# Kernel tuning notes

Measured on AMD Instinct MI355X. Metric: run time of the kernel, lower is better.

## Reference

```python
import jax, jax.numpy as jnp
import numpy as np

DIM = 192
HEADS = 6
H = 64
W = 64
B = 16
HID = int(DIM * 4.0)


def make_rope(Hh, Ww, c):
    # mirrors torch RoPE buffer: k_max = c // (2*2), angles (H,W,c//2)
    k_max = c // 4
    theta = 1.0 / (10000.0 ** (np.arange(k_max) / k_max))
    hi = np.arange(Hh)[:, None, None] * theta  # (H,1,k)
    wi = np.arange(Ww)[None, :, None] * theta  # (1,W,k)
    angles = np.concatenate([np.broadcast_to(hi, (Hh, Ww, k_max)),
                             np.broadcast_to(wi, (Hh, Ww, k_max))], axis=-1)
    return jnp.asarray(np.cos(angles), jnp.float32), jnp.asarray(np.sin(angles), jnp.float32)


def rope_apply(x, cos, sin):
    # x: (b,H,W,c); complex multiply on (re,im) pairs along last dim
    b, Hh, Ww, c = x.shape
    xr = x.reshape(b, Hh, Ww, c // 2, 2)
    re, im = xr[..., 0], xr[..., 1]
    out = jnp.stack([re * cos - im * sin, re * sin + im * cos], axis=-1)
    return out.reshape(b, Hh, Ww, c)


def dwconv(x, w, b):
    # depthwise 3x3, NCHW, kernel (C,1,3,3)
    C = x.shape[1]
    y = jax.lax.conv_general_dilated(x, w, (1, 1), 'SAME',
                                     dimension_numbers=('NCHW', 'OIHW', 'NCHW'),
                                     feature_group_count=C)
    return y + b[None, :, None, None]


def conv1x1(x, w, b):
    return jnp.einsum('bchw,oc->bohw', x, w) + b[None, :, None, None]


def ln2d(x, w, b):
    # LayerNorm over channel dim at each spatial location
    mu = x.mean(axis=1, keepdims=True)
    var = x.var(axis=1, keepdims=True)
    xn = (x - mu) / jnp.sqrt(var + 1e-5)
    return xn * w[None, :, None, None] + b[None, :, None, None]


def setup_inputs() -> dict:
    key = jax.random.key(0)
    ks = jax.random.split(key, 32)
    s = 0.02
    def p(i, shape):
        return jax.random.normal(ks[i], shape, jnp.float32) * s
    return {
        'x': jax.random.normal(ks[0], (B, DIM, H, W), jnp.float32),
        'cpe1_w': p(1, (DIM, 1, 3, 3)), 'cpe1_b': p(2, (DIM,)),
        'norm1_w': jnp.ones((DIM,), jnp.float32), 'norm1_b': jnp.zeros((DIM,), jnp.float32),
        'act_proj_w': p(3, (DIM, DIM)), 'act_proj_b': p(4, (DIM,)),
        'in_proj_w': p(5, (DIM, DIM)), 'in_proj_b': p(6, (DIM,)),
        'dwc_w': p(7, (DIM, 1, 3, 3)), 'dwc_b': p(8, (DIM,)),
        'qk_w': p(9, (2 * DIM, DIM)), 'qk_b': p(10, (2 * DIM,)),
        'lepe_w': p(11, (DIM, 1, 3, 3)), 'lepe_b': p(12, (DIM,)),
        'out_proj_w': p(13, (DIM, DIM)), 'out_proj_b': p(14, (DIM,)),
        'cpe2_w': p(15, (DIM, 1, 3, 3)), 'cpe2_b': p(16, (DIM,)),
        'norm2_w': jnp.ones((DIM,), jnp.float32), 'norm2_b': jnp.zeros((DIM,), jnp.float32),
        'fc1_w': p(17, (HID, DIM)), 'fc1_b': p(18, (HID,)),
        'fc2_w': p(19, (DIM, HID)), 'fc2_b': p(20, (DIM,)),
    }


def reference(x, cpe1_w, cpe1_b, norm1_w, norm1_b, act_proj_w, act_proj_b,
              in_proj_w, in_proj_b, dwc_w, dwc_b, qk_w, qk_b, lepe_w, lepe_b,
              out_proj_w, out_proj_b, cpe2_w, cpe2_b, norm2_w, norm2_b,
              fc1_w, fc1_b, fc2_w, fc2_b):
    b, c, Hh, Ww = x.shape
    n = Hh * Ww
    d = c // HEADS
    cos, sin = make_rope(Hh, Ww, c)

    # x = x + cpe1(x)
    x = x + dwconv(x, cpe1_w, cpe1_b)

    # MLLA block on norm1(x)
    y = ln2d(x, norm1_w, norm1_b)
    act_res = jax.nn.silu(conv1x1(y, act_proj_w, act_proj_b))
    y = conv1x1(y, in_proj_w, in_proj_b)
    t = jax.nn.silu(dwconv(y, dwc_w, dwc_b)).transpose(0, 2, 3, 1).reshape(b, n, c)

    # linear attention with ELU+1 feature map, RoPE, LePE
    qk = t @ qk_w.T + qk_b
    q = jax.nn.elu(qk[..., :c]) + 1.0
    k = jax.nn.elu(qk[..., c:]) + 1.0
    v = t
    q_rope = rope_apply(q.reshape(b, Hh, Ww, c), cos, sin).reshape(b, n, HEADS, d).transpose(0, 2, 1, 3)
    k_rope = rope_apply(k.reshape(b, Hh, Ww, c), cos, sin).reshape(b, n, HEADS, d).transpose(0, 2, 1, 3)
    qh = q.reshape(b, n, HEADS, d).transpose(0, 2, 1, 3)
    kh = k.reshape(b, n, HEADS, d).transpose(0, 2, 1, 3)
    vh = v.reshape(b, n, HEADS, d).transpose(0, 2, 1, 3)
    kmean = kh.mean(axis=2, keepdims=True)  # (b,h,1,d)
    z = 1.0 / (jnp.einsum('bhnd,bhmd->bhnm', qh, kmean) + 1e-6)  # (b,h,n,1)
    scale = n ** -0.5
    kv = jnp.einsum('bhnd,bhne->bhde', k_rope * scale, vh * scale)  # (b,h,d,d)
    attn = jnp.einsum('bhnd,bhde->bhne', q_rope, kv) * z  # (b,h,n,d)
    attn = attn.transpose(0, 2, 1, 3).reshape(b, n, c)
    v_img = vh.transpose(0, 2, 1, 3).reshape(b, Hh, Ww, c).transpose(0, 3, 1, 2)
    lepe = dwconv(v_img, lepe_w, lepe_b).transpose(0, 2, 3, 1).reshape(b, n, c)
    attn = attn + lepe

    y = attn.transpose(0, 2, 1).reshape(b, c, Hh, Ww)
    y = conv1x1(y * act_res, out_proj_w, out_proj_b)
    x = x + y

    # x = x + cpe2(x)
    x = x + dwconv(x, cpe2_w, cpe2_b)

    # MLP on norm2(x)
    y = ln2d(x, norm2_w, norm2_b)
    y = conv1x1(y, fc1_w, fc1_b)
    y = jax.nn.gelu(y, approximate=False)
    y = conv1x1(y, fc2_w, fc2_b)
    return x + y
```

## Files before the change

kernel.cpp:

```cpp
#include <hip/hip_runtime.h>
#include <hip/hip_bf16.h>

#define BQ 16
#define CH 192
#define HH 64
#define WW 64
#define HWSZ 4096
#define NPIX 65536
#define NHEADS 6
#define HDIM 32
#define NPAIR 96
#define KMAXR 48
#define HID 768

typedef __hip_bfloat16 bf16;
typedef __attribute__((ext_vector_type(8))) short short8;
typedef __attribute__((ext_vector_type(4))) float floatx4;

static __device__ __forceinline__ float b2f(bf16 v) { return __bfloat162float(v); }
static __device__ __forceinline__ bf16 f2b(float v) { return __float2bfloat16(v); }

static __device__ __forceinline__ float4 ld4(const float* p) { return *(const float4*)p; }
static __device__ __forceinline__ float4 ld4(const bf16* p) {
  uint2 u = *(const uint2*)p;
  return make_float4(__uint_as_float(u.x << 16), __uint_as_float(u.x & 0xffff0000u),
                     __uint_as_float(u.y << 16), __uint_as_float(u.y & 0xffff0000u));
}

template <int ACT>
static __device__ __forceinline__ float actf(float v) {
  if (ACT == 1) return v / (1.f + expf(-v));
  if (ACT == 2) return (v > 0.f) ? v + 1.f : expf(v);
  if (ACT == 3) return 0.5f * v * (1.f + erff(v * 0.70710678118654752f));
  return v;
}
static __device__ __forceinline__ void stv(float* p, float v) { *p = v; }
static __device__ __forceinline__ void stv(bf16* p, float v) { *p = __float2bfloat16(v); }

__global__ __launch_bounds__(256) void k_transpose_in(const float* __restrict__ in,
                                                      float* __restrict__ out) {
  __shared__ float tile[32][33];
  int c0 = blockIdx.x * 32, hw0 = blockIdx.y * 32, b = blockIdx.z;
  int tx = threadIdx.x, ty = threadIdx.y;
  const float* src = in + (size_t)b * CH * HWSZ;
  #pragma unroll
  for (int j = 0; j < 32; j += 8)
    tile[ty + j][tx] = src[(size_t)(c0 + ty + j) * HWSZ + hw0 + tx];
  __syncthreads();
  float* dst = out + (size_t)b * HWSZ * CH;
  #pragma unroll
  for (int j = 0; j < 32; j += 8)
    dst[(size_t)(hw0 + ty + j) * CH + c0 + tx] = tile[tx][ty + j];
}

__global__ __launch_bounds__(256) void k_transpose_out(const float* __restrict__ in,
                                                       float* __restrict__ out) {
  __shared__ float tile[32][33];
  int c0 = blockIdx.x * 32, hw0 = blockIdx.y * 32, b = blockIdx.z;
  int tx = threadIdx.x, ty = threadIdx.y;
  const float* src = in + (size_t)b * HWSZ * CH;
  #pragma unroll
  for (int j = 0; j < 32; j += 8)
    tile[ty + j][tx] = src[(size_t)(hw0 + ty + j) * CH + c0 + tx];
  __syncthreads();
  float* dst = out + (size_t)b * CH * HWSZ;
  #pragma unroll
  for (int j = 0; j < 32; j += 8)
    dst[(size_t)(c0 + ty + j) * HWSZ + hw0 + tx] = tile[tx][ty + j];
}

__global__ __launch_bounds__(256) void k_rope(float* __restrict__ cosT, float* __restrict__ sinT) {
  int i = blockIdx.x * 256 + threadIdx.x;
  if (i >= NPAIR * HWSZ) return;
  int hw = i & (HWSZ - 1);
  int p = i >> 12;
  int h = hw >> 6, w = hw & 63;
  int j = (p < KMAXR) ? p : p - KMAXR;
  float theta = powf(10000.f, -(float)j / (float)KMAXR);
  float pos = (p < KMAXR) ? (float)h : (float)w;
  float ang = pos * theta;
  cosT[i] = cosf(ang);
  sinT[i] = sinf(ang);
}

template <typename TI>
__global__ __launch_bounds__(192) void k_cpe_ln(const TI* __restrict__ in,
                                                const float* __restrict__ w,
                                                const float* __restrict__ bias,
                                                const float* __restrict__ g,
                                                const float* __restrict__ bt,
                                                float* __restrict__ x1o,
                                                bf16* __restrict__ yo) {
  __shared__ float grs[12][4], grq[12][4];
  int t = threadIdx.x;
  int cg = t % 48, st = t / 48;
  int c0 = cg * 4;
  int gpix = blockIdx.x * 16 + st * 4;
  int hw = gpix & (HWSZ - 1);
  int h = hw >> 6, wx = hw & 63;
  float4 w4[9];
  #pragma unroll
  for (int i = 0; i < 9; i++) w4[i] = ld4(w + c0 * 9 + i * 4);
  const float* wf = (const float*)w4;
  float4 bi = ld4(bias + c0);
  float4 acc[4];
  #pragma unroll
  for (int i = 0; i < 4; i++) acc[i] = bi;
  const TI* base = in + (size_t)gpix * CH + c0;
  #pragma unroll
  for (int dh = -1; dh <= 1; dh++) {
    bool rv = ((unsigned)(h + dh) < HH);
    float4 tap[6];
    #pragma unroll
    for (int c = 0; c < 6; c++) {
      int col = wx - 1 + c;
      bool v = rv && ((unsigned)col < WW);
      tap[c] = v ? ld4(base + (dh * WW + (c - 1)) * CH) : make_float4(0, 0, 0, 0);
    }
    #pragma unroll
    for (int i = 0; i < 4; i++) {
      #pragma unroll
      for (int dw = 0; dw < 3; dw++) {
        const int tp = (dh + 1) * 3 + dw;
        float4 tv = tap[i + dw];
        acc[i].x += tv.x * wf[0 * 9 + tp];
        acc[i].y += tv.y * wf[1 * 9 + tp];
        acc[i].z += tv.z * wf[2 * 9 + tp];
        acc[i].w += tv.w * wf[3 * 9 + tp];
      }
      if (dh == 0) {
        acc[i].x += tap[i + 1].x;
        acc[i].y += tap[i + 1].y;
        acc[i].z += tap[i + 1].z;
        acc[i].w += tap[i + 1].w;
      }
    }
  }
  float s4[4], q4[4];
  #pragma unroll
  for (int i = 0; i < 4; i++) {
    *(float4*)&x1o[(size_t)(gpix + i) * CH + c0] = acc[i];
    s4[i] = acc[i].x + acc[i].y + acc[i].z + acc[i].w;
    q4[i] = acc[i].x * acc[i].x + acc[i].y * acc[i].y + acc[i].z * acc[i].z +
            acc[i].w * acc[i].w;
  }
  #pragma unroll
  for (int m = 1; m <= 8; m <<= 1) {
    #pragma unroll
    for (int i = 0; i < 4; i++) {
      s4[i] += __shfl_xor(s4[i], m, 64);
      q4[i] += __shfl_xor(q4[i], m, 64);
    }
  }
  if ((t & 15) == 0) {
    #pragma unroll
    for (int i = 0; i < 4; i++) { grs[t >> 4][i] = s4[i]; grq[t >> 4][i] = q4[i]; }
  }
  __syncthreads();
  int s3 = st * 3;
  float4 gg = ld4(g + c0);
  float4 bb = ld4(bt + c0);
  #pragma unroll
  for (int i = 0; i < 4; i++) {
    float S = grs[s3][i] + grs[s3 + 1][i] + grs[s3 + 2][i];
    float SS = grq[s3][i] + grq[s3 + 1][i] + grq[s3 + 2][i];
    float mu = S * (1.f / CH);
    float inv = rsqrtf(SS * (1.f / CH) - mu * mu + 1e-5f);
    __align__(8) bf16 tmp[4] = {f2b((acc[i].x - mu) * inv * gg.x + bb.x),
                                f2b((acc[i].y - mu) * inv * gg.y + bb.y),
                                f2b((acc[i].z - mu) * inv * gg.z + bb.z),
                                f2b((acc[i].w - mu) * inv * gg.w + bb.w)};
    *(uint2*)&yo[(size_t)(gpix + i) * CH + c0] = *(uint2*)tmp;
  }
}

template <int MODE>
__global__ __launch_bounds__(192) void k_dwconv_strip(const bf16* __restrict__ in,
                                                      const float* __restrict__ w,
                                                      const float* __restrict__ bias,
                                                      bf16* __restrict__ out) {
  int t = threadIdx.x;
  int cg = t % 48, st = t / 48;
  int c0 = cg * 4;
  int gpix = blockIdx.x * 16 + st * 4;
  int hw = gpix & (HWSZ - 1);
  int h = hw >> 6, wx = hw & 63;
  float4 w4[9];
  #pragma unroll
  for (int i = 0; i < 9; i++) w4[i] = ld4(w + c0 * 9 + i * 4);
  const float* wf = (const float*)w4;
  float4 bi = ld4(bias + c0);
  float4 acc[4];
  #pragma unroll
  for (int i = 0; i < 4; i++) acc[i] = bi;
  const bf16* base = in + (size_t)gpix * CH + c0;
  #pragma unroll
  for (int dh = -1; dh <= 1; dh++) {
    bool rv = ((unsigned)(h + dh) < HH);
    float4 tap[6];
    #pragma unroll
    for (int c = 0; c < 6; c++) {
      int col = wx - 1 + c;
      bool v = rv && ((unsigned)col < WW);
      tap[c] = v ? ld4(base + (dh * WW + (c - 1)) * CH) : make_float4(0, 0, 0, 0);
    }
    #pragma unroll
    for (int i = 0; i < 4; i++) {
      #pragma unroll
      for (int dw = 0; dw < 3; dw++) {
        const int tp = (dh + 1) * 3 + dw;
        float4 tv = tap[i + dw];
        acc[i].x += tv.x * wf[0 * 9 + tp];
        acc[i].y += tv.y * wf[1 * 9 + tp];
        acc[i].z += tv.z * wf[2 * 9 + tp];
        acc[i].w += tv.w * wf[3 * 9 + tp];
      }
    }
  }
  #pragma unroll
  for (int i = 0; i < 4; i++) {
    bf16* op = out + (size_t)(gpix + i) * CH + c0;
    float a0 = acc[i].x, a1 = acc[i].y, a2 = acc[i].z, a3 = acc[i].w;
    if (MODE == 1) {
      a0 = a0 / (1.f + expf(-a0));
      a1 = a1 / (1.f + expf(-a1));
      a2 = a2 / (1.f + expf(-a2));
      a3 = a3 / (1.f + expf(-a3));
    } else {
      float4 cur = ld4(op);
      a0 += cur.x; a1 += cur.y; a2 += cur.z; a3 += cur.w;
    }
    __align__(8) bf16 tmp[4] = {f2b(a0), f2b(a1), f2b(a2), f2b(a3)};
    *(uint2*)op = *(uint2*)tmp;
  }
}

template <int ACT, int MULA, int RES, typename TO>
__global__ __launch_bounds__(256) void k_gemm(const bf16* __restrict__ A,
                                              const bf16* __restrict__ A2,
                                              const float* __restrict__ Wt,
                                              const float* __restrict__ bias,
                                              const float* __restrict__ Rsd,
                                              TO* __restrict__ Cout,
                                              int M, int N, int K) {
  __shared__ bf16 As[128][40];
  __shared__ bf16 Bs[64][40];
  int t = threadIdx.x;
  int wave = t >> 6, lane = t & 63;
  int quad = lane >> 4, l16 = lane & 15;
  int m0 = blockIdx.x * 128, n0 = blockIdx.y * 64;
  floatx4 acc[2][4] = {};
  for (int k0 = 0; k0 < K; k0 += 32) {
    #pragma unroll
    for (int i = 0; i < 2; i++) {
      int idx = t + i * 256;
      int m = idx >> 2, kk = (idx & 3) * 8;
      const bf16* pa = &A[(size_t)(m0 + m) * K + k0 + kk];
      if (!MULA) {
        *(short8*)&As[m][kk] = *(const short8*)pa;
      } else {
        const bf16* pb = &A2[(size_t)(m0 + m) * K + k0 + kk];
        __align__(16) bf16 tmp[8];
        #pragma unroll
        for (int j = 0; j < 8; j++) tmp[j] = f2b(b2f(pa[j]) * b2f(pb[j]));
        *(short8*)&As[m][kk] = *(const short8*)tmp;
      }
    }
    #pragma unroll
    for (int i = 0; i < 2; i++) {
      int idx = t + i * 256;
      int n = idx >> 3, kk = (idx & 7) * 4;
      float4 v = *(const float4*)&Wt[(size_t)(n0 + n) * K + k0 + kk];
      __align__(8) bf16 tmp[4] = {f2b(v.x), f2b(v.y), f2b(v.z), f2b(v.w)};
      *(uint2*)&Bs[n][kk] = *(uint2*)tmp;
    }
    __syncthreads();
    short8 af[2], bfr[4];
    #pragma unroll
    for (int i = 0; i < 2; i++)
      af[i] = *(const short8*)&As[wave * 32 + i * 16 + l16][quad * 8];
    #pragma unroll
    for (int j = 0; j < 4; j++)
      bfr[j] = *(const short8*)&Bs[j * 16 + l16][quad * 8];
    #pragma unroll
    for (int i = 0; i < 2; i++)
      #pragma unroll
      for (int j = 0; j < 4; j++)
        acc[i][j] = __builtin_amdgcn_mfma_f32_16x16x32_bf16(af[i], bfr[j], acc[i][j], 0, 0, 0);
    __syncthreads();
  }
  #pragma unroll
  for (int i = 0; i < 2; i++) {
    #pragma unroll
    for (int j = 0; j < 4; j++) {
      int n = n0 + j * 16 + l16;
      float bn = bias[n];
      #pragma unroll
      for (int r = 0; r < 4; r++) {
        int m = m0 + wave * 32 + i * 16 + quad * 4 + r;
        float v = actf<ACT>(acc[i][j][r] + bn);
        if (RES) v += Rsd[(size_t)m * N + n];
        stv(&Cout[(size_t)m * N + n], v);
      }
    }
  }
}

template <int ACTA, int ACTB, int KMEAN>
__global__ __launch_bounds__(256) void k_gemm_dual(const bf16* __restrict__ A,
                                                   const float* __restrict__ WtA,
                                                   const float* __restrict__ biasA,
                                                   const float* __restrict__ WtB,
                                                   const float* __restrict__ biasB,
                                                   bf16* __restrict__ OutA,
                                                   bf16* __restrict__ OutB,
                                                   float* __restrict__ KM,
                                                   int K) {
  __shared__ bf16 As[128][40];
  __shared__ bf16 Bs[64][40];
  __shared__ float colsum[64];
  int t = threadIdx.x;
  int wave = t >> 6, lane = t & 63;
  int quad = lane >> 4, l16 = lane & 15;
  int m0 = blockIdx.x * 128, n0 = blockIdx.y * 64;
  int half = n0 >= 192;
  int n0l = half ? n0 - 192 : n0;
  const float* Wt = half ? WtB : WtA;
  const float* bias = half ? biasB : biasA;
  bf16* Out = half ? OutB : OutA;
  if (KMEAN && half && t < 64) colsum[t] = 0.f;
  floatx4 acc[2][4] = {};
  for (int k0 = 0; k0 < K; k0 += 32) {
    #pragma unroll
    for (int i = 0; i < 2; i++) {
      int idx = t + i * 256;
      int m = idx >> 2, kk = (idx & 3) * 8;
      *(short8*)&As[m][kk] = *(const short8*)&A[(size_t)(m0 + m) * K + k0 + kk];
    }
    #pragma unroll
    for (int i = 0; i < 2; i++) {
      int idx = t + i * 256;
      int n = idx >> 3, kk = (idx & 7) * 4;
      float4 v = *(const float4*)&Wt[(size_t)(n0l + n) * K + k0 + kk];
      __align__(8) bf16 tmp[4] = {f2b(v.x), f2b(v.y), f2b(v.z), f2b(v.w)};
      *(uint2*)&Bs[n][kk] = *(uint2*)tmp;
    }
    __syncthreads();
    short8 af[2], bfr[4];
    #pragma unroll
    for (int i = 0; i < 2; i++)
      af[i] = *(const short8*)&As[wave * 32 + i * 16 + l16][quad * 8];
    #pragma unroll
    for (int j = 0; j < 4; j++)
      bfr[j] = *(const short8*)&Bs[j * 16 + l16][quad * 8];
    #pragma unroll
    for (int i = 0; i < 2; i++)
      #pragma unroll
      for (int j = 0; j < 4; j++)
        acc[i][j] = __builtin_amdgcn_mfma_f32_16x16x32_bf16(af[i], bfr[j], acc[i][j], 0, 0, 0);
    __syncthreads();
  }
  #pragma unroll
  for (int j = 0; j < 4; j++) {
    int nl = n0l + j * 16 + l16;
    float bn = bias[nl];
    float csum = 0.f;
    #pragma unroll
    for (int i = 0; i < 2; i++) {
      #pragma unroll
      for (int r = 0; r < 4; r++) {
        int m = m0 + wave * 32 + i * 16 + quad * 4 + r;
        float v = half ? actf<ACTB>(acc[i][j][r] + bn) : actf<ACTA>(acc[i][j][r] + bn);
        if (KMEAN && half) csum += v;
        Out[(size_t)m * CH + nl] = f2b(v);
      }
    }
    if (KMEAN && half) atomicAdd(&colsum[j * 16 + l16], csum);
  }
  if (KMEAN && half) {
    __syncthreads();
    if (t < 64) {
      int b = m0 >> 12;
      atomicAdd(&KM[b * CH + n0l + t], colsum[t] * (1.f / 4096.f));
    }
  }
}

__global__ __launch_bounds__(256) void k_kv(const bf16* __restrict__ k,
                                            const bf16* __restrict__ v,
                                            const float* __restrict__ cosT,
                                            const float* __restrict__ sinT,
                                            float* __restrict__ kv) {
  int bh = blockIdx.x;
  int b = bh / NHEADS, hd = bh % NHEADS;
  int chunk0 = blockIdx.y * 512;
  __shared__ bf16 ks[256][40];
  __shared__ bf16 vs[256][40];
  int t = threadIdx.x;
  int d = t >> 3;
  int e0 = (t & 7) * 4;
  float a0 = 0, a1 = 0, a2 = 0, a3 = 0;
  for (int sub = 0; sub < 2; sub++) {
    int n0 = chunk0 + sub * 256;
    #pragma unroll
    for (int it = 0; it < 4; it++) {
      int idx = t + it * 256;
      int row = idx >> 2, c0 = (idx & 3) * 8;
      int n = n0 + row;
      size_t gi = ((size_t)(b * HWSZ + n)) * CH + hd * HDIM + c0;
      *(short8*)&vs[row][c0] = *(const short8*)&v[gi];
      float4 klo = ld4(&k[gi]);
      float4 khi = ld4(&k[gi + 4]);
      int prb = hd * 16 + (c0 >> 1);
      float cs0 = cosT[(size_t)(prb + 0) * HWSZ + n];
      float sn0 = sinT[(size_t)(prb + 0) * HWSZ + n];
      float cs1 = cosT[(size_t)(prb + 1) * HWSZ + n];
      float sn1 = sinT[(size_t)(prb + 1) * HWSZ + n];
      float cs2 = cosT[(size_t)(prb + 2) * HWSZ + n];
      float sn2 = sinT[(size_t)(prb + 2) * HWSZ + n];
      float cs3 = cosT[(size_t)(prb + 3) * HWSZ + n];
      float sn3 = sinT[(size_t)(prb + 3) * HWSZ + n];
      __align__(16) bf16 kt[8];
      kt[0] = f2b(klo.x * cs0 - klo.y * sn0);
      kt[1] = f2b(klo.x * sn0 + klo.y * cs0);
      kt[2] = f2b(klo.z * cs1 - klo.w * sn1);
      kt[3] = f2b(klo.z * sn1 + klo.w * cs1);
      kt[4] = f2b(khi.x * cs2 - khi.y * sn2);
      kt[5] = f2b(khi.x * sn2 + khi.y * cs2);
      kt[6] = f2b(khi.z * cs3 - khi.w * sn3);
      kt[7] = f2b(khi.z * sn3 + khi.w * cs3);
      *(short8*)&ks[row][c0] = *(const short8*)kt;
    }
    __syncthreads();
    #pragma unroll 4
    for (int i = 0; i < 256; i++) {
      float kd = b2f(ks[i][d]);
      float4 vv = ld4(&vs[i][e0]);
      a0 += kd * vv.x;
      a1 += kd * vv.y;
      a2 += kd * vv.z;
      a3 += kd * vv.w;
    }
    __syncthreads();
  }
  float* dst = kv + (size_t)bh * (HDIM * HDIM) + d * HDIM + e0;
  const float sc = 1.f / 4096.f;
  atomicAdd(dst + 0, a0 * sc);
  atomicAdd(dst + 1, a1 * sc);
  atomicAdd(dst + 2, a2 * sc);
  atomicAdd(dst + 3, a3 * sc);
}

__global__ __launch_bounds__(256) void k_attn(const bf16* __restrict__ q,
                                              const float* __restrict__ kv,
                                              const float* __restrict__ kmean,
                                              const float* __restrict__ cosT,
                                              const float* __restrict__ sinT,
                                              bf16* __restrict__ attn) {
  int hd = blockIdx.y, b = blockIdx.z;
  int hw = blockIdx.x * 256 + threadIdx.x;
  int bh = b * NHEADS + hd;
  __shared__ float kvs[32][33];
  __shared__ float kms[32];
  #pragma unroll
  for (int i = 0; i < 4; i++) {
    int idx = threadIdx.x + i * 256;
    kvs[idx >> 5][idx & 31] = kv[(size_t)bh * 1024 + idx];
  }
  if (threadIdx.x < 32) kms[threadIdx.x] = kmean[b * CH + hd * HDIM + threadIdx.x];
  __syncthreads();
  int pix = b * HWSZ + hw;
  const bf16* qp = q + (size_t)pix * CH + hd * HDIM;
  float qv[32];
  #pragma unroll
  for (int i = 0; i < 32; i++) qv[i] = b2f(qp[i]);
  float z = 1e-6f;
  #pragma unroll
  for (int d = 0; d < 32; d++) z += qv[d] * kms[d];
  float o[32] = {};
  #pragma unroll
  for (int p = 0; p < 16; p++) {
    float cs = cosT[(size_t)(hd * 16 + p) * HWSZ + hw];
    float sn = sinT[(size_t)(hd * 16 + p) * HWSZ + hw];
    float re = qv[2 * p], im = qv[2 * p + 1];
    float qr = re * cs - im * sn;
    float qi = re * sn + im * cs;
    #pragma unroll
    for (int e = 0; e < 32; e++)
      o[e] += qr * kvs[2 * p][e] + qi * kvs[2 * p + 1][e];
  }
  float zi = 1.f / z;
  bf16* op = attn + (size_t)pix * CH + hd * HDIM;
  #pragma unroll
  for (int i = 0; i < 4; i++) {
    __align__(16) bf16 tmp[8];
    #pragma unroll
    for (int j = 0; j < 8; j++) tmp[j] = f2b(o[i * 8 + j] * zi);
    *(short8*)&op[i * 8] = *(const short8*)tmp;
  }
}

extern "C" void kernel_launch(void* const* d_in, const int* in_sizes, int n_in,
                              void* d_out, int out_size, void* d_ws, size_t ws_size,
                              hipStream_t stream) {
  const float* x = (const float*)d_in[0];
  const float* cpe1w = (const float*)d_in[1];
  const float* cpe1b = (const float*)d_in[2];
  const float* n1w = (const float*)d_in[3];
  const float* n1b = (const float*)d_in[4];
  const float* apw = (const float*)d_in[5];
  const float* apb = (const float*)d_in[6];
  const float* ipw = (const float*)d_in[7];
  const float* ipb = (const float*)d_in[8];
  const float* dwcw = (const float*)d_in[9];
  const float* dwcb = (const float*)d_in[10];
  const float* qkw = (const float*)d_in[11];
  const float* qkb = (const float*)d_in[12];
  const float* lepw = (const float*)d_in[13];
  const float* lepb = (const float*)d_in[14];
  const float* opw = (const float*)d_in[15];
  const float* opb = (const float*)d_in[16];
  const float* cpe2w = (const float*)d_in[17];
  const float* cpe2b = (const float*)d_in[18];
  const float* n2w = (const float*)d_in[19];
  const float* n2b = (const float*)d_in[20];
  const float* f1w = (const float*)d_in[21];
  const float* f1b = (const float*)d_in[22];
  const float* f2w = (const float*)d_in[23];
  const float* f2b = (const float*)d_in[24];
  float* out = (float*)d_out;

  float* ws = (float*)d_ws;
  const size_t S = (size_t)NPIX * CH;
  float* FA = ws;
  float* FB = ws + S;
  bf16* barena = (bf16*)(ws + 2 * S);
  bf16* b0 = barena;
  bf16* b1 = barena + S;
  bf16* b2 = barena + 2 * S;
  bf16* KB = (bf16*)FA;
  float* COS = ws + 2 * S + 3 * S / 2;
  float* SIN = COS + (size_t)NPAIR * HWSZ;
  float* KV = SIN + (size_t)NPAIR * HWSZ;
  float* KM = KV + BQ * NHEADS * HDIM * HDIM;
  bf16* HIDB = (bf16*)FB;

  dim3 tb(32, 8);
  k_transpose_in<<<dim3(6, 128, BQ), tb, 0, stream>>>(x, FA);
  k_rope<<<dim3(NPAIR * HWSZ / 256), dim3(256), 0, stream>>>(COS, SIN);
  k_cpe_ln<float><<<dim3(NPIX / 16), dim3(192), 0, stream>>>(FA, cpe1w, cpe1b, n1w, n1b, FB, b0);
  k_gemm_dual<1, 0, 0><<<dim3(NPIX / 128, 6), dim3(256), 0, stream>>>(
      b0, apw, apb, ipw, ipb, b1, b2, nullptr, CH);
  k_dwconv_strip<1><<<dim3(NPIX / 16), dim3(192), 0, stream>>>(b2, dwcw, dwcb, b0);
  hipMemsetAsync(KM, 0, (size_t)BQ * CH * sizeof(float), stream);
  k_gemm_dual<2, 2, 1><<<dim3(NPIX / 128, 6), dim3(256), 0, stream>>>(
      b0, qkw, qkb, qkw + CH * CH, qkb + CH, b2, KB, KM, CH);
  hipMemsetAsync(KV, 0, (size_t)BQ * NHEADS * HDIM * HDIM * sizeof(float), stream);
  k_kv<<<dim3(BQ * NHEADS, 8), dim3(256), 0, stream>>>(KB, b0, COS, SIN, KV);
  k_attn<<<dim3(HWSZ / 256, NHEADS, BQ), dim3(256), 0, stream>>>(b2, KV, KM, COS, SIN, KB);
  k_dwconv_strip<2><<<dim3(NPIX / 16), dim3(192), 0, stream>>>(b0, lepw, lepb, KB);
  k_gemm<0, 1, 1, bf16><<<dim3(NPIX / 128, 3), dim3(256), 0, stream>>>(
      KB, b1, opw, opb, FB, b2, NPIX, CH, CH);
  k_cpe_ln<bf16><<<dim3(NPIX / 16), dim3(192), 0, stream>>>(b2, cpe2w, cpe2b, n2w, n2b, FA, b0);
  for (int s = 0; s < 2; s++) {
    size_t off = (size_t)s * (NPIX / 2) * CH;
    k_gemm<3, 0, 0, bf16><<<dim3((NPIX / 2) / 128, HID / 64), dim3(256), 0, stream>>>(
        b0 + off, (const bf16*)nullptr, f1w, f1b, (const float*)nullptr, HIDB, NPIX / 2, HID, CH);
    k_gemm<0, 0, 1, float><<<dim3((NPIX / 2) / 128, 3), dim3(256), 0, stream>>>(
        HIDB, (const bf16*)nullptr, f2w, f2b, FA + off, FA + off, NPIX / 2, CH, HID);
  }
  k_transpose_out<<<dim3(6, 128, BQ), tb, 0, stream>>>(FA, out);
}
```

Before: 633.9 us.

## Pre-convert weights to bf16 once and stage full 192-wide K chunks in GEMMs

Adds a kernel that converts all linear weights to bf16 in workspace once per call, so GEMMs load bf16 weights directly instead of converting fp32 per tile. The GEMM kernels now stage 192-wide K slices into LDS (the whole K for dual GEMMs) and run six MFMA steps per barrier, cutting syncs and load-loop overhead. LDS per block grows to about 77 KB, which may lower occupancy, and one extra small kernel launch is added.

Result: no change. 637.3 us (+0.5%).

```diff
diff --git a/kernel.cpp b/kernel.cpp
--- a/kernel.cpp
+++ b/kernel.cpp
@@ -81,6 +81,29 @@
   float ang = pos * theta;
   cosT[i] = cosf(ang);
   sinT[i] = sinf(ang);
+}
+
+#define WTOT 479232
+__global__ __launch_bounds__(256) void k_wcvt(const float* __restrict__ ap,
+                                              const float* __restrict__ ip,
+                                              const float* __restrict__ qk,
+                                              const float* __restrict__ op,
+                                              const float* __restrict__ f1,
+                                              const float* __restrict__ f2,
+                                              bf16* __restrict__ o) {
+  int i = (blockIdx.x * 256 + threadIdx.x) * 4;
+  if (i >= WTOT) return;
+  const float* src;
+  int off;
+  if (i < 36864)       { src = ap; off = 0; }
+  else if (i < 73728)  { src = ip; off = 36864; }
+  else if (i < 147456) { src = qk; off = 73728; }
+  else if (i < 184320) { src = op; off = 147456; }
+  else if (i < 331776) { src = f1; off = 184320; }
+  else                 { src = f2; off = 331776; }
+  float4 v = ld4(src + (i - off));
+  __align__(8) bf16 t4[4] = {f2b(v.x), f2b(v.y), f2b(v.z), f2b(v.w)};
+  *(uint2*)&o[i] = *(uint2*)t4;
 }
 
 template <typename TI>
@@ -238,55 +261,56 @@
 template <int ACT, int MULA, int RES, typename TO>
 __global__ __launch_bounds__(256) void k_gemm(const bf16* __restrict__ A,
                                               const bf16* __restrict__ A2,
-                                              const float* __restrict__ Wt,
+                                              const bf16* __restrict__ Wt,
                                               const float* __restrict__ bias,
                                               const float* __restrict__ Rsd,
                                               TO* __restrict__ Cout,
                                               int M, int N, int K) {
-  __shared__ bf16 As[128][40];
-  __shared__ bf16 Bs[64][40];
+  __shared__ bf16 As[128][200];
+  __shared__ bf16 Bs[64][200];
   int t = threadIdx.x;
   int wave = t >> 6, lane = t & 63;
   int quad = lane >> 4, l16 = lane & 15;
   int m0 = blockIdx.x * 128, n0 = blockIdx.y * 64;
   floatx4 acc[2][4] = {};
-  for (int k0 = 0; k0 < K; k0 += 32) {
-    #pragma unroll
-    for (int i = 0; i < 2; i++) {
+  for (int kc = 0; kc < K; kc += 192) {
+    #pragma unroll
+    for (int i = 0; i < 12; i++) {
       int idx = t + i * 256;
-      int m = idx >> 2, kk = (idx & 3) * 8;
-      const bf16* pa = &A[(size_t)(m0 + m) * K + k0 + kk];
+      int m = idx / 24, ck = (idx % 24) * 8;
+      const bf16* pa = &A[(size_t)(m0 + m) * K + kc + ck];
       if (!MULA) {
-        *(short8*)&As[m][kk] = *(const short8*)pa;
+        *(short8*)&As[m][ck] = *(const short8*)pa;
       } else {
-        const bf16* pb = &A2[(size_t)(m0 + m) * K + k0 + kk];
+        const bf16* pb = &A2[(size_t)(m0 + m) * K + kc + ck];
         __align__(16) bf16 tmp[8];
         #pragma unroll
         for (int j = 0; j < 8; j++) tmp[j] = f2b(b2f(pa[j]) * b2f(pb[j]));
-        *(short8*)&As[m][kk] = *(const short8*)tmp;
+        *(short8*)&As[m][ck] = *(const short8*)tmp;
       }
     }
     #pragma unroll
-    for (int i = 0; i < 2; i++) {
+    for (int i = 0; i < 6; i++) {
       int idx = t + i * 256;
-      int n = idx >> 3, kk = (idx & 7) * 4;
-      float4 v = *(const float4*)&Wt[(size_t)(n0 + n) * K + k0 + kk];
-      __align__(8) bf16 tmp[4] = {f2b(v.x), f2b(v.y), f2b(v.z), f2b(v.w)};
-      *(uint2*)&Bs[n][kk] = *(uint2*)tmp;
+      int n = idx / 24, ck = (idx % 24) * 8;
+      *(short8*)&Bs[n][ck] = *(const short8*)&Wt[(size_t)(n0 + n) * K + kc + ck];
     }
     __syncthreads();
-    short8 af[2], bfr[4];
-    #pragma unroll
-    for (int i = 0; i < 2; i++)
-      af[i] = *(const short8*)&As[wave * 32 + i * 16 + l16][quad * 8];
-    #pragma unroll
-    for (int j = 0; j < 4; j++)
-      bfr[j] = *(const short8*)&Bs[j * 16 + l16][quad * 8];
-    #pragma unroll
-    for (int i = 0; i < 2; i++)
+    #pragma unroll
+    for (int ks = 0; ks < 6; ks++) {
+      short8 af[2], bfr[4];
+      #pragma unroll
+      for (int i = 0; i < 2; i++)
+        af[i] = *(const short8*)&As[wave * 32 + i * 16 + l16][ks * 32 + quad * 8];
       #pragma unroll
       for (int j = 0; j < 4; j++)
-        acc[i][j] = __builtin_amdgcn_mfma_f32_16x16x32_bf16(af[i], bfr[j], acc[i][j], 0, 0, 0);
+        bfr[j] = *(const short8*)&Bs[j * 16 + l16][ks * 32 + quad * 8];
+      #pragma unroll
+      for (int i = 0; i < 2; i++)
+        #pragma unroll
+        for (int j = 0; j < 4; j++)
+          acc[i][j] = __builtin_amdgcn_mfma_f32_16x16x32_bf16(af[i], bfr[j], acc[i][j], 0, 0, 0);
+    }
     __syncthreads();
   }
   #pragma unroll
@@ -308,16 +332,16 @@
 
 template <int ACTA, int ACTB, int KMEAN>
 __global__ __launch_bounds__(256) void k_gemm_dual(const bf16* __restrict__ A,
-                                                   const float* __restrict__ WtA,
+                                                   const bf16* __restrict__ WtA,
                                                    const float* __restrict__ biasA,
-                                                   const float* __restrict__ WtB,
+                                                   const bf16* __restrict__ WtB,
                                                    const float* __restrict__ biasB,
                                                    bf16* __restrict__ OutA,
                                                    bf16* __restrict__ OutB,
                                                    float* __restrict__ KM,
                                                    int K) {
-  __shared__ bf16 As[128][40];
-  __shared__ bf16 Bs[64][40];
+  __shared__ bf16 As[128][200];
+  __shared__ bf16 Bs[64][200];
   __shared__ float colsum[64];
   int t = threadIdx.x;
   int wave = t >> 6, lane = t & 63;
@@ -325,40 +349,38 @@
   int m0 = blockIdx.x * 128, n0 = blockIdx.y * 64;
   int half = n0 >= 192;
   int n0l = half ? n0 - 192 : n0;
-  const float* Wt = half ? WtB : WtA;
+  const bf16* Wt = half ? WtB : WtA;
   const float* bias = half ? biasB : biasA;
   bf16* Out = half ? OutB : OutA;
   if (KMEAN && half && t < 64) colsum[t] = 0.f;
   floatx4 acc[2][4] = {};
-  for (int k0 = 0; k0 < K; k0 += 32) {
-    #pragma unroll
-    for (int i = 0; i < 2; i++) {
-      int idx = t + i * 256;
-      int m = idx >> 2, kk = (idx & 3) * 8;
-      *(short8*)&As[m][kk] = *(const short8*)&A[(size_t)(m0 + m) * K + k0 + kk];
-    }
-    #pragma unroll
-    for (int i = 0; i < 2; i++) {
-      int idx = t + i * 256;
-      int n = idx >> 3, kk = (idx & 7) * 4;
-      float4 v = *(const float4*)&Wt[(size_t)(n0l + n) * K + k0 + kk];
-      __align__(8) bf16 tmp[4] = {f2b(v.x), f2b(v.y), f2b(v.z), f2b(v.w)};
-      *(uint2*)&Bs[n][kk] = *(uint2*)tmp;
-    }
-    __syncthreads();
+  #pragma unroll
+  for (int i = 0; i < 12; i++) {
+    int idx = t + i * 256;
+    int m = idx / 24, ck = (idx % 24) * 8;
+    *(short8*)&As[m][ck] = *(const short8*)&A[(size_t)(m0 + m) * CH + ck];
+  }
+  #pragma unroll
+  for (int i = 0; i < 6; i++) {
+    int idx = t + i * 256;
+    int n = idx / 24, ck = (idx % 24) * 8;
+    *(short8*)&Bs[n][ck] = *(const short8*)&Wt[(size_t)(n0l + n) * CH + ck];
+  }
+  __syncthreads();
+  #pragma unroll
+  for (int ks = 0; ks < 6; ks++) {
     short8 af[2], bfr[4];
     #pragma unroll
     for (int i = 0; i < 2; i++)
-      af[i] = *(const short8*)&As[wave * 32 + i * 16 + l16][quad * 8];
+      af[i] = *(const short8*)&As[wave * 32 + i * 16 + l16][ks * 32 + quad * 8];
     #pragma unroll
     for (int j = 0; j < 4; j++)
-      bfr[j] = *(const short8*)&Bs[j * 16 + l16][quad * 8];
+      bfr[j] = *(const short8*)&Bs[j * 16 + l16][ks * 32 + quad * 8];
     #pragma unroll
     for (int i = 0; i < 2; i++)
       #pragma unroll
       for (int j = 0; j < 4; j++)
         acc[i][j] = __builtin_amdgcn_mfma_f32_16x16x32_bf16(af[i], bfr[j], acc[i][j], 0, 0, 0);
-    __syncthreads();
   }
   #pragma unroll
   for (int j = 0; j < 4; j++) {
@@ -543,31 +565,40 @@
   float* SIN = COS + (size_t)NPAIR * HWSZ;
   float* KV = SIN + (size_t)NPAIR * HWSZ;
   float* KM = KV + BQ * NHEADS * HDIM * HDIM;
+  bf16* WB = (bf16*)(KM + BQ * CH);
+  bf16* apw16 = WB;
+  bf16* ipw16 = WB + 36864;
+  bf16* qkw16 = WB + 73728;
+  bf16* opw16 = WB + 147456;
+  bf16* f1w16 = WB + 184320;
+  bf16* f2w16 = WB + 331776;
   bf16* HIDB = (bf16*)FB;
 
   dim3 tb(32, 8);
+  k_wcvt<<<dim3((WTOT / 4 + 255) / 256), dim3(256), 0, stream>>>(
+      apw, ipw, qkw, opw, f1w, f2w, WB);
   k_transpose_in<<<dim3(6, 128, BQ), tb, 0, stream>>>(x, FA);
   k_rope<<<dim3(NPAIR * HWSZ / 256), dim3(256), 0, stream>>>(COS, SIN);
   k_cpe_ln<float><<<dim3(NPIX / 16), dim3(192), 0, stream>>>(FA, cpe1w, cpe1b, n1w, n1b, FB, b0);
   k_gemm_dual<1, 0, 0><<<dim3(NPIX / 128, 6), dim3(256), 0, stream>>>(
-      b0, apw, apb, ipw, ipb, b1, b2, nullptr, CH);
+      b0, apw16, apb, ipw16, ipb, b1, b2, nullptr, CH);
   k_dwconv_strip<1><<<dim3(NPIX / 16), dim3(192), 0, stream>>>(b2, dwcw, dwcb, b0);
   hipMemsetAsync(KM, 0, (size_t)BQ * CH * sizeof(float), stream);
   k_gemm_dual<2, 2, 1><<<dim3(NPIX / 128, 6), dim3(256), 0, stream>>>(
-      b0, qkw, qkb, qkw + CH * CH, qkb + CH, b2, KB, KM, CH);
+      b0, qkw16, qkb, qkw16 + CH * CH, qkb + CH, b2, KB, KM, CH);
   hipMemsetAsync(KV, 0, (size_t)BQ * NHEADS * HDIM * HDIM * sizeof(float), stream);
   k_kv<<<dim3(BQ * NHEADS, 8), dim3(256), 0, stream>>>(KB, b0, COS, SIN, KV);
   k_attn<<<dim3(HWSZ / 256, NHEADS, BQ), dim3(256), 0, stream>>>(b2, KV, KM, COS, SIN, KB);
   k_dwconv_strip<2><<<dim3(NPIX / 16), dim3(192), 0, stream>>>(b0, lepw, lepb, KB);
   k_gemm<0, 1, 1, bf16><<<dim3(NPIX / 128, 3), dim3(256), 0, stream>>>(
-      KB, b1, opw, opb, FB, b2, NPIX, CH, CH);
+      KB, b1, opw16, opb, FB, b2, NPIX, CH, CH);
   k_cpe_ln<bf16><<<dim3(NPIX / 16), dim3(192), 0, stream>>>(b2, cpe2w, cpe2b, n2w, n2b, FA, b0);
   for (int s = 0; s < 2; s++) {
     size_t off = (size_t)s * (NPIX / 2) * CH;
     k_gemm<3, 0, 0, bf16><<<dim3((NPIX / 2) / 128, HID / 64), dim3(256), 0, stream>>>(
-        b0 + off, (const bf16*)nullptr, f1w, f1b, (const float*)nullptr, HIDB, NPIX / 2, HID, CH);
+        b0 + off, (const bf16*)nullptr, f1w16, f1b, (const float*)nullptr, HIDB, NPIX / 2, HID, CH);
     k_gemm<0, 0, 1, float><<<dim3((NPIX / 2) / 128, 3), dim3(256), 0, stream>>>(
-        HIDB, (const bf16*)nullptr, f2w, f2b, FA + off, FA + off, NPIX / 2, CH, HID);
+        HIDB, (const bf16*)nullptr, f2w16, f2b, FA + off, FA + off, NPIX / 2, CH, HID);
   }
   k_transpose_out<<<dim3(6, 128, BQ), tb, 0, stream>>>(FA, out);
 }
```
